# Kernel tuning notes

Measured on AMD Instinct MI355X. Metric: run time of the kernel, lower is better.

The kernel has to match this reference:

```python
import jax, jax.numpy as jnp
import numpy as np

D_KQ = 1024  # output_key_query_dim, used for the 1/sqrt(d) scale


def setup_inputs() -> dict:
    key = jax.random.key(0)
    kx, kq, kk, kv = jax.random.split(key, 4)
    B, S, D = 4, 2048, 1024
    x = jax.random.normal(kx, (B, S, D), dtype=jnp.float32)
    # nn.Linear(in, out, bias=False) weights, shape (out, in); y = x @ W.T
    scale = 1.0 / np.sqrt(D)
    Wq = jax.random.normal(kq, (D_KQ, D), dtype=jnp.float32) * scale
    Wk = jax.random.normal(kk, (D_KQ, D), dtype=jnp.float32) * scale
    Wv = jax.random.normal(kv, (D, D), dtype=jnp.float32) * scale
    return {"x": x, "Wq": Wq, "Wk": Wk, "Wv": Wv}


def reference(x, Wq, Wk, Wv):
    # q, k, v projections (bias=False): y = x @ W.T
    q = jnp.einsum('bsd,ed->bse', x, Wq)  # [B,S,Dkq]
    k = jnp.einsum('bsd,ed->bse', x, Wk)  # [B,S,Dkq]
    v = jnp.einsum('bsd,ed->bse', x, Wv)  # [B,S,Dv]
    scores = jnp.einsum('bqe,bke->bqk', q, k) / jnp.sqrt(
        jnp.asarray(D_KQ, dtype=q.dtype))
    # NOTE: the original torch code's masked_fill(causal_mask == 1, -inf) is a
    # no-op because the buffer contains only {-inf, 0} values, never 1.
    # Faithfully, NO causal mask is applied.
    attn = jax.nn.softmax(scores, axis=-1)
    # dropout in eval mode -> identity
    out = jnp.einsum('bqk,bke->bqe', attn, v)  # [B,S,Dv]
    return out
```

## Files before the change

### kernel.cpp

```cpp
#include <hip/hip_runtime.h>
#include <stdint.h>

#define B_ 4
#define S_ 2048
#define D_ 1024

typedef __attribute__((ext_vector_type(8))) short short8;
typedef __attribute__((ext_vector_type(4))) float f32x4;
typedef __attribute__((ext_vector_type(4))) int int4v;

__device__ inline ushort f2bf(float f) {
  union { float f; uint32_t u; } v; v.f = f;
  uint32_t u = v.u;
  u += 0x7FFFu + ((u >> 16) & 1u);
  return (ushort)(u >> 16);
}

__device__ inline float bf2f(ushort u) {
  union { uint32_t u; float f; } c; c.u = ((uint32_t)u) << 16;
  return c.f;
}

__device__ inline void gload_lds16(const ushort* g, ushort* l) {
  __builtin_amdgcn_global_load_lds(
      (__attribute__((address_space(1))) void*)(uintptr_t)g,
      (__attribute__((address_space(3))) void*)(uintptr_t)l,
      16, 0, 0);
}

__device__ inline uint lds_off(const ushort* p) {
  return (uint)(uintptr_t)(const __attribute__((address_space(3))) ushort*)(uintptr_t)p;
}

__device__ inline short8 dsr128(uint addr) {
  int4v r;
  asm volatile("ds_read_b128 %0, %1" : "=v"(r) : "v"(addr));
  return __builtin_bit_cast(short8, r);
}

__device__ inline void vwaitN(int n) {
  switch (n) {
    case 0: asm volatile("s_waitcnt vmcnt(0)"); break;
    case 1: asm volatile("s_waitcnt vmcnt(1)"); break;
    case 2: asm volatile("s_waitcnt vmcnt(2)"); break;
    case 3: asm volatile("s_waitcnt vmcnt(3)"); break;
    case 4: asm volatile("s_waitcnt vmcnt(4)"); break;
    case 5: asm volatile("s_waitcnt vmcnt(5)"); break;
    case 6: asm volatile("s_waitcnt vmcnt(6)"); break;
    case 7: asm volatile("s_waitcnt vmcnt(7)"); break;
    default: asm volatile("s_waitcnt vmcnt(8)"); break;
  }
}

__device__ inline void abar() { asm volatile("s_barrier"); }

__device__ inline void lgkm0() {
  asm volatile("s_waitcnt lgkmcnt(0)");
  __builtin_amdgcn_sched_barrier(0);
}

__global__ __launch_bounds__(256) void convert_all(
    const float* __restrict__ x, const float* __restrict__ wq,
    const float* __restrict__ wk, const float* __restrict__ wv,
    ushort* __restrict__ xb, ushort* __restrict__ wcat) {
  const int NX = B_ * S_ * D_;
  const int NW = D_ * D_;
  int e = (blockIdx.x * 256 + threadIdx.x) * 4;
  const float* src;
  ushort* dst;
  if (e < NX) {
    src = x + e; dst = xb + e;
  } else {
    int e2 = e - NX;
    int w = e2 / NW, off = e2 - w * NW;
    src = (w == 0 ? wq : w == 1 ? wk : wv) + off;
    dst = wcat + e2;
  }
  float4 f = *(const float4*)src;
  ushort4 o;
  o.x = f2bf(f.x); o.y = f2bf(f.y); o.z = f2bf(f.z); o.w = f2bf(f.w);
  *(ushort4*)dst = o;
}


template <int H, int BM, int BN>
__device__ inline void mfma_ph(short8 (&afv)[BM / 64], short8 (&bfv)[BN / 64],
                               f32x4 (&acc)[BM / 32][BN / 64]) {
  constexpr int J = BM / 64, NF = BN / 64;
  __builtin_amdgcn_s_setprio(1);
  #pragma unroll
  for (int j = 0; j < J; ++j)
    #pragma unroll
    for (int nf = 0; nf < NF; ++nf)
      acc[H * J + j][nf] = __builtin_amdgcn_mfma_f32_16x16x32_bf16(
          afv[j], bfv[nf], acc[H * J + j][nf], 0, 0, 0);
  __builtin_amdgcn_s_setprio(0);
}

template <int BM, int BN, bool OUT_BF16, bool V_TRANS>
__global__ __launch_bounds__(512, 2) void gemm_p(
    const ushort* __restrict__ A, const ushort* __restrict__ Bm,
    void* __restrict__ C, ushort* __restrict__ Vt,
    int N, int K, int lda, int ldb, int ldc,
    long sA, long sB, long sC, float scale) {
  constexpr int J = BM / 64, NF = BN / 64, MF = BM / 32;
  constexpr int LAH = BM / 128;
  constexpr int LBH = BN / 128;
  constexpr int ABUF = BM * 64;
  constexpr int BBUF = BN * 64;
  constexpr int VW1 = 2 * LAH + 2 * LBH;
  __shared__ ushort lds[2 * ABUF + 3 * BBUF];
  ushort* ldsA = lds;
  ushort* ldsB = lds + 2 * ABUF;

  const int tid = threadIdx.x;
  const int wid = tid >> 6, lane = tid & 63;
  const int wr = wid >> 2, wc = wid & 3;
  const int la = lane & 15, kg = lane >> 4;
  const int m0 = blockIdx.x * BM, n0 = blockIdx.y * BN;
  const int bz = blockIdx.z;
  const ushort* Ag = A + (size_t)bz * sA;
  const ushort* Bg = Bm + (size_t)bz * sB;

  uint aOff[2][LAH]; int aDst[2][LAH];
  #pragma unroll
  for (int h = 0; h < 2; ++h)
    #pragma unroll
    for (int l = 0; l < LAH; ++l) {
      int li = l * 512 + tid, ridx = li >> 3, c = li & 7;
      int row = (ridx < BM / 4) ? h * (BM / 4) + ridx
                                : (h + 2) * (BM / 4) + (ridx - BM / 4);
      int gc = c ^ (row & 7);
      aOff[h][l] = (uint)((m0 + row) * lda + gc * 8);
      aDst[h][l] = row * 64 + c * 8;
    }
  uint bOff[2][LBH]; int bDst[2][LBH];
  #pragma unroll
  for (int h = 0; h < 2; ++h)
    #pragma unroll
    for (int l = 0; l < LBH; ++l) {
      int li = l * 512 + tid, ridx = li >> 3, c = li & 7;
      int row = h * (BN / 2) + ridx;
      int gc = c ^ (row & 7);
      bOff[h][l] = (uint)((n0 + row) * ldb + gc * 8);
      bDst[h][l] = row * 64 + c * 8;
    }

  auto stageA = [&](int h, int buf, int t) {
    #pragma unroll
    for (int l = 0; l < LAH; ++l)
      gload_lds16(Ag + aOff[h][l] + (size_t)t * 64, ldsA + buf * ABUF + aDst[h][l]);
  };
  auto stageB = [&](int h, int slot, int t) {
    #pragma unroll
    for (int l = 0; l < LBH; ++l)
      gload_lds16(Bg + bOff[h][l] + (size_t)t * 64, ldsB + slot * BBUF + bDst[h][l]);
  };

  uint offA[2][2][J];
  #pragma unroll
  for (int h = 0; h < 2; ++h)
    #pragma unroll
    for (int ks = 0; ks < 2; ++ks)
      #pragma unroll
      for (int j = 0; j < J; ++j) {
        int row = wr * (BM / 2) + h * (BM / 4) + j * 16 + la;
        int kc = ((ks * 4 + kg) ^ (row & 7)) * 8;
        offA[h][ks][j] = (uint)((row * 64 + kc) * 2);
      }
  uint offB[2][NF];
  #pragma unroll
  for (int ks = 0; ks < 2; ++ks)
    #pragma unroll
    for (int nf = 0; nf < NF; ++nf) {
      int row = wc * (BN / 4) + nf * 16 + la;
      int kc = ((ks * 4 + kg) ^ (row & 7)) * 8;
      offB[ks][nf] = (uint)((row * 64 + kc) * 2);
    }
  const uint ldsA0 = lds_off(ldsA);
  const uint ldsB0 = lds_off(ldsB);

  f32x4 acc[MF][NF];
  #pragma unroll
  for (int m = 0; m < MF; ++m)
    #pragma unroll
    for (int n = 0; n < NF; ++n) acc[m][n] = (f32x4)(0.f);
  short8 af[J], bf0[NF], bf1[NF];

  const int NT = K / 64;

  stageA(0, 0, 0); stageB(0, 0, 0); stageB(1, 0, 0);
  stageA(1, 0, 0);
  stageA(0, 1, 1); stageB(0, 1, 1); stageB(1, 1, 1);

  int bs = 0;
  for (int t = 0; t < NT; ++t) {
    const uint aB = ldsA0 + (uint)((t & 1) * ABUF * 2);
    const uint bB = ldsB0 + (uint)(bs * BBUF * 2);
    const int bs2 = (bs == 0) ? 2 : bs - 1;

    vwaitN(t + 1 < NT ? VW1 : LAH);
    abar();
    #pragma unroll
    for (int j = 0; j < J; ++j) af[j] = dsr128(aB + offA[0][0][j]);
    #pragma unroll
    for (int nf = 0; nf < NF; ++nf) bf0[nf] = dsr128(bB + offB[0][nf]);
    if (t + 1 < NT) stageA(1, (t + 1) & 1, t + 1);
    lgkm0();
    mfma_ph<0, BM, BN>(af, bf0, acc);
    #pragma unroll
    for (int j = 0; j < J; ++j) af[j] = dsr128(aB + offA[0][1][j]);
    #pragma unroll
    for (int nf = 0; nf < NF; ++nf) bf1[nf] = dsr128(bB + offB[1][nf]);
    lgkm0();
    mfma_ph<0, BM, BN>(af, bf1, acc);

    vwaitN(t + 1 < NT ? VW1 : 0);
    abar();
    #pragma unroll
    for (int j = 0; j < J; ++j) af[j] = dsr128(aB + offA[1][0][j]);
    if (t + 2 < NT) { stageA(0, t & 1, t + 2); stageB(0, bs2, t + 2); }
    lgkm0();
    mfma_ph<1, BM, BN>(af, bf0, acc);
    #pragma unroll
    for (int j = 0; j < J; ++j) af[j] = dsr128(aB + offA[1][1][j]);
    if (t + 2 < NT) stageB(1, bs2, t + 2);
    lgkm0();
    mfma_ph<1, BM, BN>(af, bf1, acc);

    bs = (bs == 2) ? 0 : bs + 1;
  }

  if (V_TRANS && n0 >= 2048) {
    const int b = m0 >> 11;
    ushort* Vb = Vt + (size_t)b * D_ * S_;
    #pragma unroll
    for (int m = 0; m < MF; ++m) {
      #pragma unroll
      for (int n = 0; n < NF; ++n) {
        int r = m0 + wr * (BM / 2) + m * 16 + kg * 4;
        int e = (n0 - 2048) + wc * (BN / 4) + n * 16 + la;
        int s0 = r & 2047;
        ushort4 o;
        o.x = f2bf(acc[m][n][0]); o.y = f2bf(acc[m][n][1]);
        o.z = f2bf(acc[m][n][2]); o.w = f2bf(acc[m][n][3]);
        *(ushort4*)&Vb[(size_t)e * S_ + s0] = o;
      }
    }
  } else {
    char* Cb = (char*)C;
    #pragma unroll
    for (int m = 0; m < MF; ++m) {
      #pragma unroll
      for (int n = 0; n < NF; ++n) {
        int r = m0 + wr * (BM / 2) + m * 16 + kg * 4;
        int col = n0 + wc * (BN / 4) + n * 16 + la;
        #pragma unroll
        for (int jj = 0; jj < 4; ++jj) {
          float v = acc[m][n][jj] * scale;
          size_t idx = (size_t)bz * sC + (size_t)(r + jj) * ldc + col;
          if (OUT_BF16) ((ushort*)Cb)[idx] = f2bf(v);
          else          ((float*)Cb)[idx]  = v;
        }
      }
    }
  }
}

__global__ __launch_bounds__(256) void softmax_rows(
    const ushort* __restrict__ Sc, ushort* __restrict__ P) {
  size_t row = blockIdx.x;
  const ushort* src = Sc + row * S_;
  ushort* dst = P + row * S_;
  int tid = threadIdx.x;
  short8 v = *(const short8*)(src + tid * 8);
  float vals[8];
  float m = -1e30f;
  #pragma unroll
  for (int i = 0; i < 8; ++i) {
    vals[i] = bf2f((ushort)v[i]);
    m = fmaxf(m, vals[i]);
  }
  #pragma unroll
  for (int off = 1; off < 64; off <<= 1) m = fmaxf(m, __shfl_xor(m, off));
  __shared__ float redm[4];
  if ((tid & 63) == 0) redm[tid >> 6] = m;
  __syncthreads();
  m = fmaxf(fmaxf(redm[0], redm[1]), fmaxf(redm[2], redm[3]));
  float s = 0.f;
  #pragma unroll
  for (int i = 0; i < 8; ++i) {
    vals[i] = __expf(vals[i] - m);
    s += vals[i];
  }
  #pragma unroll
  for (int off = 1; off < 64; off <<= 1) s += __shfl_xor(s, off);
  __shared__ float reds[4];
  if ((tid & 63) == 0) reds[tid >> 6] = s;
  __syncthreads();
  s = reds[0] + reds[1] + reds[2] + reds[3];
  float inv = 1.0f / s;
  short8 o;
  #pragma unroll
  for (int i = 0; i < 8; ++i) o[i] = (short)f2bf(vals[i] * inv);
  *(short8*)(dst + tid * 8) = o;
}

extern "C" void kernel_launch(void* const* d_in, const int* in_sizes, int n_in,
                              void* d_out, int out_size, void* d_ws, size_t ws_size,
                              hipStream_t stream) {
  const float* x  = (const float*)d_in[0];
  const float* Wq = (const float*)d_in[1];
  const float* Wk = (const float*)d_in[2];
  const float* Wv = (const float*)d_in[3];
  float* out = (float*)d_out;

  char* ws = (char*)d_ws;
  ushort* Xb   = (ushort*)(ws + 0);
  ushort* Wcat = (ushort*)(ws + 16777216);
  ushort* QKV  = (ushort*)(ws + 23068672);
  ushort* Vt   = (ushort*)(ws + 73400320);
  ushort* Sc   = (ushort*)(ws + 90177536);
  ushort* P    = (ushort*)(ws + 157286400);

  const int NTOT = B_ * S_ * D_ + 3 * D_ * D_;

  convert_all<<<NTOT / 4 / 256, 256, 0, stream>>>(x, Wq, Wk, Wv, Xb, Wcat);

  gemm_p<128, 256, true, true><<<dim3(64, 12, 1), 512, 0, stream>>>(
      Xb, Wcat, QKV, Vt, 3072, 1024, 1024, 1024, 3072, 0, 0, 0, 1.0f);

  gemm_p<128, 256, true, false><<<dim3(16, 8, B_), 512, 0, stream>>>(
      QKV, QKV + 1024, Sc, nullptr, 2048, 1024, 3072, 3072, 2048,
      (long)S_ * 3072, (long)S_ * 3072, (long)S_ * S_, 1.0f / 32.0f);

  softmax_rows<<<B_ * S_, 256, 0, stream>>>(Sc, P);

  gemm_p<128, 256, false, false><<<dim3(16, 4, B_), 512, 0, stream>>>(
      P, Vt, out, nullptr, 1024, 2048, 2048, 2048, 1024,
      (long)S_ * S_, (long)S_ * D_, (long)S_ * D_, 1.0f);
}
```

Measured before the change: 175.0 us.

## Add 256x256-tile GEMM kernel for QKV projection and score GEMMs

```diff
diff --git a/kernel.cpp b/kernel.cpp
--- a/kernel.cpp
+++ b/kernel.cpp
@@ -83,6 +83,181 @@
 }
 
 
+template <int HH, int NH>
+__device__ inline void mfma16(short8 (&af)[4][2], short8 (&bf)[2][2][2],
+                              f32x4 (&acc)[8][4]) {
+  __builtin_amdgcn_s_setprio(1);
+  #pragma unroll
+  for (int mf = 0; mf < 4; ++mf)
+    #pragma unroll
+    for (int nf = 0; nf < 2; ++nf)
+      #pragma unroll
+      for (int ks = 0; ks < 2; ++ks)
+        acc[HH * 4 + mf][NH * 2 + nf] = __builtin_amdgcn_mfma_f32_16x16x32_bf16(
+            af[mf][ks], bf[NH][nf][ks], acc[HH * 4 + mf][NH * 2 + nf], 0, 0, 0);
+  __builtin_amdgcn_s_setprio(0);
+}
+
+template <bool V_TRANS>
+__global__ __launch_bounds__(512, 2) void gemm256(
+    const ushort* __restrict__ A, const ushort* __restrict__ Bm,
+    ushort* __restrict__ C, ushort* __restrict__ Vt,
+    int K, int lda, int ldb, int ldc,
+    long sA, long sB, long sC, float scale) {
+  constexpr int ATILE = 256 * 64;
+  __shared__ ushort lds[4 * ATILE];
+  ushort* ldsA = lds;
+  ushort* ldsB = lds + 2 * ATILE;
+
+  const int tid = threadIdx.x;
+  const int wid = tid >> 6, lane = tid & 63;
+  const int wr = wid >> 2, wc = wid & 3;
+  const int la = lane & 15, kg = lane >> 4;
+  const int m0 = blockIdx.x * 256, n0 = blockIdx.y * 256;
+  const int bz = blockIdx.z;
+  const ushort* Ag = A + (size_t)bz * sA;
+  const ushort* Bg = Bm + (size_t)bz * sB;
+
+  uint aOff[2][2]; int aDst[2][2];
+  uint bOff[2][2]; int bDst[2][2];
+  #pragma unroll
+  for (int h = 0; h < 2; ++h)
+    #pragma unroll
+    for (int l = 0; l < 2; ++l) {
+      int li = l * 512 + tid, ridx = li >> 3, c = li & 7;
+      int rowA = (ridx < 64) ? h * 64 + ridx : 128 + h * 64 + (ridx - 64);
+      int gcA = c ^ (rowA & 7);
+      aOff[h][l] = (uint)((m0 + rowA) * lda + gcA * 8);
+      aDst[h][l] = rowA * 64 + c * 8;
+      int rowB = (ridx >> 5) * 64 + h * 32 + (ridx & 31);
+      int gcB = c ^ (rowB & 7);
+      bOff[h][l] = (uint)((n0 + rowB) * ldb + gcB * 8);
+      bDst[h][l] = rowB * 64 + c * 8;
+    }
+
+  auto stageA = [&](int h, int buf, int t) {
+    #pragma unroll
+    for (int l = 0; l < 2; ++l)
+      gload_lds16(Ag + aOff[h][l] + (size_t)t * 64, ldsA + buf * ATILE + aDst[h][l]);
+  };
+  auto stageB = [&](int h, int buf, int t) {
+    #pragma unroll
+    for (int l = 0; l < 2; ++l)
+      gload_lds16(Bg + bOff[h][l] + (size_t)t * 64, ldsB + buf * ATILE + bDst[h][l]);
+  };
+
+  uint offAq[2][2][4];
+  #pragma unroll
+  for (int hh = 0; hh < 2; ++hh)
+    #pragma unroll
+    for (int ks = 0; ks < 2; ++ks)
+      #pragma unroll
+      for (int mf = 0; mf < 4; ++mf) {
+        int row = wr * 128 + hh * 64 + mf * 16 + la;
+        int kc = ((ks * 4 + kg) ^ (row & 7)) * 8;
+        offAq[hh][ks][mf] = (uint)((row * 64 + kc) * 2);
+      }
+  uint offBq[2][2][2];
+  #pragma unroll
+  for (int nh = 0; nh < 2; ++nh)
+    #pragma unroll
+    for (int ks = 0; ks < 2; ++ks)
+      #pragma unroll
+      for (int nf = 0; nf < 2; ++nf) {
+        int row = wc * 64 + nh * 32 + nf * 16 + la;
+        int kc = ((ks * 4 + kg) ^ (row & 7)) * 8;
+        offBq[nh][ks][nf] = (uint)((row * 64 + kc) * 2);
+      }
+  const uint ldsA0 = lds_off(ldsA);
+  const uint ldsB0 = lds_off(ldsB);
+
+  f32x4 acc[8][4];
+  #pragma unroll
+  for (int m = 0; m < 8; ++m)
+    #pragma unroll
+    for (int n = 0; n < 4; ++n) acc[m][n] = (f32x4)(0.f);
+  short8 af[4][2];
+  short8 bf[2][2][2];
+
+  const int NT = K / 64;
+
+  stageA(0, 0, 0); stageB(0, 0, 0); stageB(1, 0, 0); stageA(1, 0, 0);
+
+  for (int t = 0; t < NT; ++t) {
+    const uint aB = ldsA0 + (uint)((t & 1) * ATILE * 2);
+    const uint bB = ldsB0 + (uint)((t & 1) * ATILE * 2);
+    const int nb = (t + 1) & 1;
+
+    vwaitN(4);
+    abar();
+    #pragma unroll
+    for (int mf = 0; mf < 4; ++mf)
+      #pragma unroll
+      for (int ks = 0; ks < 2; ++ks) af[mf][ks] = dsr128(aB + offAq[0][ks][mf]);
+    #pragma unroll
+    for (int nf = 0; nf < 2; ++nf)
+      #pragma unroll
+      for (int ks = 0; ks < 2; ++ks) bf[0][nf][ks] = dsr128(bB + offBq[0][ks][nf]);
+    if (t + 1 < NT) stageA(0, nb, t + 1);
+    lgkm0();
+    mfma16<0, 0>(af, bf, acc);
+
+    vwaitN(t + 1 < NT ? 4 : 2);
+    abar();
+    #pragma unroll
+    for (int nf = 0; nf < 2; ++nf)
+      #pragma unroll
+      for (int ks = 0; ks < 2; ++ks) bf[1][nf][ks] = dsr128(bB + offBq[1][ks][nf]);
+    if (t + 1 < NT) stageB(0, nb, t + 1);
+    lgkm0();
+    mfma16<0, 1>(af, bf, acc);
+
+    vwaitN(t + 1 < NT ? 4 : 0);
+    abar();
+    #pragma unroll
+    for (int mf = 0; mf < 4; ++mf)
+      #pragma unroll
+      for (int ks = 0; ks < 2; ++ks) af[mf][ks] = dsr128(aB + offAq[1][ks][mf]);
+    if (t + 1 < NT) stageB(1, nb, t + 1);
+    lgkm0();
+    mfma16<1, 0>(af, bf, acc);
+
+    if (t + 1 < NT) stageA(1, nb, t + 1);
+    mfma16<1, 1>(af, bf, acc);
+  }
+
+  if (V_TRANS && n0 >= 2048) {
+    const int b = m0 >> 11;
+    ushort* Vb = Vt + (size_t)b * D_ * S_;
+    #pragma unroll
+    for (int mf = 0; mf < 8; ++mf) {
+      #pragma unroll
+      for (int nf = 0; nf < 4; ++nf) {
+        int r = m0 + wr * 128 + (mf >> 2) * 64 + (mf & 3) * 16 + kg * 4;
+        int e = (n0 - 2048) + wc * 64 + (nf >> 1) * 32 + (nf & 1) * 16 + la;
+        int s0 = r & 2047;
+        ushort4 o;
+        o.x = f2bf(acc[mf][nf][0]); o.y = f2bf(acc[mf][nf][1]);
+        o.z = f2bf(acc[mf][nf][2]); o.w = f2bf(acc[mf][nf][3]);
+        *(ushort4*)&Vb[(size_t)e * S_ + s0] = o;
+      }
+    }
+  } else {
+    #pragma unroll
+    for (int mf = 0; mf < 8; ++mf) {
+      #pragma unroll
+      for (int nf = 0; nf < 4; ++nf) {
+        int r = m0 + wr * 128 + (mf >> 2) * 64 + (mf & 3) * 16 + kg * 4;
+        int col = n0 + wc * 64 + (nf >> 1) * 32 + (nf & 1) * 16 + la;
+        #pragma unroll
+        for (int jj = 0; jj < 4; ++jj)
+          C[(size_t)bz * sC + (size_t)(r + jj) * ldc + col] =
+              f2bf(acc[mf][nf][jj] * scale);
+      }
+    }
+  }
+}
+
 template <int H, int BM, int BN>
 __device__ inline void mfma_ph(short8 (&afv)[BM / 64], short8 (&bfv)[BN / 64],
                                f32x4 (&acc)[BM / 32][BN / 64]) {
@@ -97,11 +272,10 @@
   __builtin_amdgcn_s_setprio(0);
 }
 
-template <int BM, int BN, bool OUT_BF16, bool V_TRANS>
+template <int BM, int BN, bool OUT_BF16>
 __global__ __launch_bounds__(512, 2) void gemm_p(
     const ushort* __restrict__ A, const ushort* __restrict__ Bm,
-    void* __restrict__ C, ushort* __restrict__ Vt,
-    int N, int K, int lda, int ldb, int ldc,
+    void* __restrict__ C, int N, int K, int lda, int ldb, int ldc,
     long sA, long sB, long sC, float scale) {
   constexpr int J = BM / 64, NF = BN / 64, MF = BM / 32;
   constexpr int LAH = BM / 128;
@@ -231,37 +405,19 @@
     bs = (bs == 2) ? 0 : bs + 1;
   }
 
-  if (V_TRANS && n0 >= 2048) {
-    const int b = m0 >> 11;
-    ushort* Vb = Vt + (size_t)b * D_ * S_;
-    #pragma unroll
-    for (int m = 0; m < MF; ++m) {
-      #pragma unroll
-      for (int n = 0; n < NF; ++n) {
-        int r = m0 + wr * (BM / 2) + m * 16 + kg * 4;
-        int e = (n0 - 2048) + wc * (BN / 4) + n * 16 + la;
-        int s0 = r & 2047;
-        ushort4 o;
-        o.x = f2bf(acc[m][n][0]); o.y = f2bf(acc[m][n][1]);
-        o.z = f2bf(acc[m][n][2]); o.w = f2bf(acc[m][n][3]);
-        *(ushort4*)&Vb[(size_t)e * S_ + s0] = o;
-      }
-    }
-  } else {
-    char* Cb = (char*)C;
-    #pragma unroll
-    for (int m = 0; m < MF; ++m) {
-      #pragma unroll
-      for (int n = 0; n < NF; ++n) {
-        int r = m0 + wr * (BM / 2) + m * 16 + kg * 4;
-        int col = n0 + wc * (BN / 4) + n * 16 + la;
-        #pragma unroll
-        for (int jj = 0; jj < 4; ++jj) {
-          float v = acc[m][n][jj] * scale;
-          size_t idx = (size_t)bz * sC + (size_t)(r + jj) * ldc + col;
-          if (OUT_BF16) ((ushort*)Cb)[idx] = f2bf(v);
-          else          ((float*)Cb)[idx]  = v;
-        }
+  char* Cb = (char*)C;
+  #pragma unroll
+  for (int m = 0; m < MF; ++m) {
+    #pragma unroll
+    for (int n = 0; n < NF; ++n) {
+      int r = m0 + wr * (BM / 2) + m * 16 + kg * 4;
+      int col = n0 + wc * (BN / 4) + n * 16 + la;
+      #pragma unroll
+      for (int jj = 0; jj < 4; ++jj) {
+        float v = acc[m][n][jj] * scale;
+        size_t idx = (size_t)bz * sC + (size_t)(r + jj) * ldc + col;
+        if (OUT_BF16) ((ushort*)Cb)[idx] = f2bf(v);
+        else          ((float*)Cb)[idx]  = v;
       }
     }
   }
@@ -327,16 +483,16 @@
 
   convert_all<<<NTOT / 4 / 256, 256, 0, stream>>>(x, Wq, Wk, Wv, Xb, Wcat);
 
-  gemm_p<128, 256, true, true><<<dim3(64, 12, 1), 512, 0, stream>>>(
-      Xb, Wcat, QKV, Vt, 3072, 1024, 1024, 1024, 3072, 0, 0, 0, 1.0f);
-
-  gemm_p<128, 256, true, false><<<dim3(16, 8, B_), 512, 0, stream>>>(
-      QKV, QKV + 1024, Sc, nullptr, 2048, 1024, 3072, 3072, 2048,
+  gemm256<true><<<dim3(32, 12, 1), 512, 0, stream>>>(
+      Xb, Wcat, QKV, Vt, 1024, 1024, 1024, 3072, 0, 0, 0, 1.0f);
+
+  gemm256<false><<<dim3(8, 8, B_), 512, 0, stream>>>(
+      QKV, QKV + 1024, Sc, nullptr, 1024, 3072, 3072, 2048,
       (long)S_ * 3072, (long)S_ * 3072, (long)S_ * S_, 1.0f / 32.0f);
 
   softmax_rows<<<B_ * S_, 256, 0, stream>>>(Sc, P);
 
-  gemm_p<128, 256, false, false><<<dim3(16, 4, B_), 512, 0, stream>>>(
-      P, Vt, out, nullptr, 1024, 2048, 2048, 2048, 1024,
+  gemm_p<128, 256, false><<<dim3(16, 4, B_), 512, 0, stream>>>(
+      P, Vt, out, 1024, 2048, 2048, 2048, 1024,
       (long)S_ * S_, (long)S_ * D_, (long)S_ * D_, 1.0f);
 }
```

After: 167.9 us. 4.0% less time.
